# Kernel optimization log

Hardware: AMD Instinct MI355X
Metric: run time of the kernel (lower is better)

## Reference

```python
import jax, jax.numpy as jnp
import numpy as np

N_QUBITS = 8
N_LAYERS = 2
CDT = jnp.complex64


def _apply_1q(state, U, w):
    # state: [B] + [2]*n complex; U: [B,2,2] complex; acts on wire w (axis w+1)
    s = jnp.moveaxis(state, w + 1, -1)
    s = jnp.einsum('b...i,bji->b...j', s, U)
    return jnp.moveaxis(s, -1, w + 1)


def _rx(theta):
    t = theta * 0.5
    c, s = jnp.cos(t).astype(CDT), jnp.sin(t).astype(CDT)
    return jnp.stack([jnp.stack([c, -1j * s], -1), jnp.stack([-1j * s, c], -1)], -2)


def _ry(theta):
    t = theta * 0.5
    c, s = jnp.cos(t).astype(CDT), jnp.sin(t).astype(CDT)
    return jnp.stack([jnp.stack([c, -s], -1), jnp.stack([s, c], -1)], -2)


def _rz(theta):
    e = jnp.exp(-0.5j * theta.astype(CDT))
    z = jnp.zeros_like(e)
    return jnp.stack([jnp.stack([e, z], -1), jnp.stack([z, jnp.conj(e)], -1)], -2)


def _cnot(state, c, t):
    # control wire c, target wire t (c < t in this circuit) -> axes c+1, t+1
    s0 = jnp.take(state, jnp.array([0]), axis=c + 1)
    s1 = jnp.take(state, jnp.array([1]), axis=c + 1)
    s1 = jnp.flip(s1, axis=t + 1)
    return jnp.concatenate([s0, s1], axis=c + 1)


def _circuit(x, params):
    n, L = N_QUBITS, N_LAYERS
    B = x.shape[0]
    state = jnp.zeros((B,) + (2,) * n, CDT).at[(slice(None),) + (0,) * n].set(1.0)
    # data encoding: RY(x_i * pi), per-sample angles
    for i in range(n):
        state = _apply_1q(state, _ry(x[:, i] * jnp.pi), i)
    n_rot, n_ent = 3 * n, n * (n - 1) // 2
    for l in range(L):
        base = l * (n_rot + n_ent)
        rot = params[base:base + n_rot]
        ent = params[base + n_rot:base + n_rot + n_ent]
        for i in range(n):
            state = _apply_1q(state, _rx(jnp.broadcast_to(rot[3 * i], (B,))), i)
            state = _apply_1q(state, _ry(jnp.broadcast_to(rot[3 * i + 1], (B,))), i)
            state = _apply_1q(state, _rz(jnp.broadcast_to(rot[3 * i + 2], (B,))), i)
        k = 0
        for i in range(n):
            for j in range(i + 1, n):
                state = _cnot(state, i, j)
                state = _apply_1q(state, _rz(jnp.broadcast_to(ent[k], (B,))), j)
                k += 1
    probs = state.real ** 2 + state.imag ** 2  # [B] + [2]*n
    ev = []
    for w in range(n):
        p = jnp.moveaxis(probs, w + 1, 1).reshape(B, 2, -1).sum(-1)
        ev.append(p[:, 0] - p[:, 1])  # <Z_w>
    return jnp.stack(ev, -1)  # [B, n_qubits]


def setup_inputs() -> dict:
    key = jax.random.key(0)
    k1, k2, k3, k4 = jax.random.split(key, 4)
    B, n, C = 4096, N_QUBITS, 10
    x = jax.random.uniform(k1, (B, n), dtype=jnp.float32)
    params = jax.random.normal(k2, (104,), dtype=jnp.float32) * 0.1
    W = jax.random.normal(k3, (C, n), dtype=jnp.float32) * (1.0 / np.sqrt(n))
    b = jax.random.normal(k4, (C,), dtype=jnp.float32) * 0.01
    return {"x": x, "params": params, "W": W, "b": b}


def reference(x, params, W, b):
    quantum_out = _circuit(x, params)          # [B, n_qubits]
    return quantum_out @ W.T + b               # Linear post-process, [B, n_classes]
```

## Files before the change

kernel.cpp:

```cpp
#include <hip/hip_runtime.h>


#define PI_HALF 1.57079632679489662f

__device__ __forceinline__ float shfx(float v, int m)      { return __shfl_xor(v, m, 64); }
__device__ __forceinline__ float shfl_from(float v, int l) { return __shfl(v, l, 64); }
__device__ __forceinline__ float rdlane(float v, int l) {
    return __int_as_float(__builtin_amdgcn_readlane(__float_as_int(v), l));
}
__device__ __forceinline__ float sgnterm(float th, int pword) {
    return __int_as_float(__float_as_int(-th) ^ (int)((unsigned)pword << 31));
}

__global__ __launch_bounds__(256) void vqc_fused(
    const float* __restrict__ x,
    const float* __restrict__ prm,
    const float* __restrict__ W,
    const float* __restrict__ bvec,
    float* __restrict__ out)
{
    const int lane = threadIdx.x & 63;
    const int bi = __builtin_amdgcn_readfirstlane((blockIdx.x << 2) + (threadIdx.x >> 6));

    float mar, mai, mbr, mbi;
    {
        const int t = lane & 15;
        const int l = t >> 3, q = t & 7;
        const float* p3 = prm + l * 52 + 3 * q;
        float cx, sx, cy, sy, cz, sz;
        __sincosf(p3[0] * 0.5f, &sx, &cx);
        __sincosf(p3[1] * 0.5f, &sy, &cy);
        __sincosf(p3[2] * 0.5f, &sz, &cz);
        float n00r =  cy * cx, n00i =  sy * sx;
        float n01r = -sy * cx, n01i = -cy * sx;
        mar = cz * n00r + sz * n00i;
        mai = cz * n00i - sz * n00r;
        mbr = cz * n01r + sz * n01i;
        mbi = cz * n01i - sz * n01r;
    }

    float cw[8], swv[8];
    {
        const float4 x0 = ((const float4*)(x + bi * 8))[0];
        const float4 x1 = ((const float4*)(x + bi * 8))[1];
        float xv[8] = {x0.x, x0.y, x0.z, x0.w, x1.x, x1.y, x1.z, x1.w};
        #pragma unroll
        for (int w = 0; w < 8; ++w)
            __sincosf(xv[w] * PI_HALF, &swv[w], &cw[w]);
    }
    float base = 1.f;
    #pragma unroll
    for (int w = 0; w < 6; ++w)
        base *= ((lane >> (5 - w)) & 1) ? swv[w] : cw[w];
    float re[4], im[4];
    re[0] = base * cw[6]  * cw[7];  re[1] = base * cw[6]  * swv[7];
    re[2] = base * swv[6] * cw[7];  re[3] = base * swv[6] * swv[7];
    im[0] = im[1] = im[2] = im[3] = 0.f;

    int lb[6];
    #pragma unroll
    for (int b = 0; b < 6; ++b) lb[b] = lane >> b;

    const int pr = __popc(lane) & 1;
    int g = lane; g ^= g >> 1; g ^= g >> 2; g ^= g >> 4;
    const int src_lane = g;

    #pragma unroll
    for (int l = 0; l < 2; ++l) {
        #pragma unroll
        for (int i = 0; i < 8; ++i) {
            const int srcl = l * 8 + i;
            const float ar  = rdlane(mar, srcl);
            const float ai  = rdlane(mai, srcl);
            const float br  = rdlane(mbr, srcl);
            const float bi_ = rdlane(mbi, srcl);
            const int p = 7 - i;
            if (p >= 2) {
                const int mk = 1 << (p - 2);
                const int h  = (lane >> (p - 2)) & 1;
                const float Ai = h ? -ai : ai;
                const float Br = h ? -br : br;
                #pragma unroll
                for (int r = 0; r < 4; ++r) {
                    float pre = shfx(re[r], mk), pim = shfx(im[r], mk);
                    float cr = re[r], ci = im[r];
                    re[r] = ar * cr - Ai * ci + Br * pre - bi_ * pim;
                    im[r] = ar * ci + Ai * cr + Br * pim + bi_ * pre;
                }
            } else if (p == 1) {
                #pragma unroll
                for (int r0i = 0; r0i < 2; ++r0i) {
                    const int i0 = r0i, i1 = r0i + 2;
                    float r0 = re[i0], i0v = im[i0], r1 = re[i1], i1v = im[i1];
                    re[i0] =  ar * r0 - ai * i0v + br * r1 - bi_ * i1v;
                    im[i0] =  ar * i0v + ai * r0 + br * i1v + bi_ * r1;
                    re[i1] = -br * r0 - bi_ * i0v + ar * r1 + ai * i1v;
                    im[i1] = -br * i0v + bi_ * r0 + ar * i1v - ai * r1;
                }
            } else {
                #pragma unroll
                for (int r0i = 0; r0i < 2; ++r0i) {
                    const int i0 = 2 * r0i, i1 = 2 * r0i + 1;
                    float r0 = re[i0], i0v = im[i0], r1 = re[i1], i1v = im[i1];
                    re[i0] =  ar * r0 - ai * i0v + br * r1 - bi_ * i1v;
                    im[i0] =  ar * i0v + ai * r0 + br * i1v + bi_ * r1;
                    re[i1] = -br * r0 - bi_ * i0v + ar * r1 + ai * i1v;
                    im[i1] = -br * i0v + bi_ * r0 + ar * i1v - ai * r1;
                }
            }
        }

        {
            const float* pb = prm + l * 52 + 24;
            float A = 0.f, B6 = 0.f, B7 = 0.f, T = 0.f;
            int k = 0;
            #pragma unroll
            for (int i = 0; i < 8; ++i) {
                #pragma unroll
                for (int j = i + 1; j < 8; ++j, ++k) {
                    const float th = pb[k];
                    if (j <= 5)      A  += sgnterm(th, lb[5 - i] ^ lb[5 - j]);
                    else if (i == 6) T   = th;
                    else if (j == 6) B6 += sgnterm(th, lb[5 - i]);
                    else             B7 += sgnterm(th, lb[5 - i]);
                }
            }
            const float AB  = A + B6, AmB = A - B6;
            const float BmT = B7 - T, BpT = B7 + T;
            float ph[4] = { 0.5f * (AB  + BmT), 0.5f * (AB  - BmT),
                            0.5f * (AmB + BpT), 0.5f * (AmB - BpT) };
            #pragma unroll
            for (int r = 0; r < 4; ++r) {
                float c, s;
                __sincosf(ph[r], &s, &c);
                float nr = c * re[r] - s * im[r];
                float ni = c * im[r] + s * re[r];
                re[r] = nr; im[r] = ni;
            }
        }

        if (l == 0) {
            float Bre[4], Bim[4];
            #pragma unroll
            for (int m = 0; m < 4; ++m) {
                Bre[m] = shfl_from(re[m], src_lane);
                Bim[m] = shfl_from(im[m], src_lane);
            }
            re[0] = pr ? Bre[3] : Bre[0];  im[0] = pr ? Bim[3] : Bim[0];
            re[1] = pr ? Bre[2] : Bre[1];  im[1] = pr ? Bim[2] : Bim[1];
            re[2] = pr ? Bre[0] : Bre[3];  im[2] = pr ? Bim[0] : Bim[3];
            re[3] = pr ? Bre[1] : Bre[2];  im[3] = pr ? Bim[1] : Bim[2];
        }
    }

    float p0 = re[0]*re[0] + im[0]*im[0];
    float p1 = re[1]*re[1] + im[1]*im[1];
    float p2 = re[2]*re[2] + im[2]*im[2];
    float p3 = re[3]*re[3] + im[3]*im[3];
    float psum = p0 + p1 + p2 + p3;

    float v = psum;
    #pragma unroll
    for (int m = 1; m < 64; m <<= 1) {
        float pp = shfx(v, m);
        v = (lane & m) ? (pp - v) : (v + pp);
    }
    float t6 = p0 + p1 - p2 - p3;  t6 = (lane & 1) ? -t6 : t6;
    float t7 = p0 - p1 - p2 + p3;
    #pragma unroll
    for (int m = 1; m < 64; m <<= 1) { t6 += shfx(t6, m); t7 += shfx(t7, m); }

    const float e0 = shfl_from(v, 32);
    const float e1 = shfl_from(v, 48);
    const float e2 = shfl_from(v, 24);
    const float e3 = shfl_from(v, 12);
    const float e4 = shfl_from(v, 6);
    const float e5 = shfl_from(v, 3);

    if (lane < 10) {
        const float* Wr = W + lane * 8;
        float acc = bvec[lane];
        acc += e0 * Wr[0] + e1 * Wr[1] + e2 * Wr[2] + e3 * Wr[3];
        acc += e4 * Wr[4] + e5 * Wr[5] + t6 * Wr[6] + t7 * Wr[7];
        out[bi * 10 + lane] = acc;
    }
}

extern "C" void kernel_launch(void* const* d_in, const int* in_sizes, int n_in,
                              void* d_out, int out_size, void* d_ws, size_t ws_size,
                              hipStream_t stream) {
    const float* x    = (const float*)d_in[0];
    const float* prm  = (const float*)d_in[1];
    const float* W    = (const float*)d_in[2];
    const float* bvec = (const float*)d_in[3];
    float* out = (float*)d_out;

    const int B = in_sizes[0] / 8;
    vqc_fused<<<B / 4, 256, 0, stream>>>(x, prm, W, bvec, out);
}
```

Measured before the change: 14.19 us.

## Process two samples per wavefront using packed FP32 complex arithmetic

Each wavefront now simulates two batch samples instead of one, so the grid is halved. Complex amplitudes are held as float2 pairs and the gate updates use v_pk_mul_f32/v_pk_fma_f32 inline asm with op_sel swizzles, doing real and imaginary parts in one instruction. Gate-matrix readlanes, parameter sin/cos and the entangling-phase setup are amortized over two samples. In exchange each thread uses more registers, and fewer blocks means less parallelism across the GPU.

```diff
diff --git a/kernel.cpp b/kernel.cpp
--- a/kernel.cpp
+++ b/kernel.cpp
@@ -1,15 +1,38 @@
 #include <hip/hip_runtime.h>
 
+
+typedef float v2f __attribute__((ext_vector_type(2)));
 
 #define PI_HALF 1.57079632679489662f
 
 __device__ __forceinline__ float shfx(float v, int m)      { return __shfl_xor(v, m, 64); }
 __device__ __forceinline__ float shfl_from(float v, int l) { return __shfl(v, l, 64); }
+__device__ __forceinline__ v2f shfx2(v2f z, int m) {
+    v2f r; r.x = shfx(z.x, m); r.y = shfx(z.y, m); return r;
+}
+__device__ __forceinline__ v2f shfl_from2(v2f z, int l) {
+    v2f r; r.x = shfl_from(z.x, l); r.y = shfl_from(z.y, l); return r;
+}
 __device__ __forceinline__ float rdlane(float v, int l) {
     return __int_as_float(__builtin_amdgcn_readlane(__float_as_int(v), l));
 }
 __device__ __forceinline__ float sgnterm(float th, int pword) {
     return __int_as_float(__float_as_int(-th) ^ (int)((unsigned)pword << 31));
+}
+
+__device__ __forceinline__ v2f pk_mul(v2f a, v2f b) {
+    v2f d; asm("v_pk_mul_f32 %0, %1, %2" : "=v"(d) : "v"(a), "v"(b)); return d;
+}
+__device__ __forceinline__ v2f pk_fma(v2f a, v2f b, v2f c) {
+    v2f d; asm("v_pk_fma_f32 %0, %1, %2, %3" : "=v"(d) : "v"(a), "v"(b), "v"(c)); return d;
+}
+__device__ __forceinline__ v2f pk_fma_sw1(v2f a, v2f b, v2f c) {
+    v2f d; asm("v_pk_fma_f32 %0, %1, %2, %3 op_sel:[0,1,0] op_sel_hi:[1,0,1]"
+               : "=v"(d) : "v"(a), "v"(b), "v"(c)); return d;
+}
+__device__ __forceinline__ v2f pk_fma_sw01(v2f a, v2f b, v2f c) {
+    v2f d; asm("v_pk_fma_f32 %0, %1, %2, %3 op_sel:[1,1,0] op_sel_hi:[0,0,1]"
+               : "=v"(d) : "v"(a), "v"(b), "v"(c)); return d;
 }
 
 __global__ __launch_bounds__(256) void vqc_fused(
@@ -20,7 +43,9 @@
     float* __restrict__ out)
 {
     const int lane = threadIdx.x & 63;
-    const int bi = __builtin_amdgcn_readfirstlane((blockIdx.x << 2) + (threadIdx.x >> 6));
+    const int wid  = __builtin_amdgcn_readfirstlane((int)(threadIdx.x >> 6));
+    const int bi0  = (blockIdx.x << 3) + (wid << 1);
+    const int bi1  = bi0 + 1;
 
     float mar, mai, mbr, mbi;
     {
@@ -39,23 +64,28 @@
         mbi = cz * n01i - sz * n01r;
     }
 
-    float cw[8], swv[8];
-    {
-        const float4 x0 = ((const float4*)(x + bi * 8))[0];
-        const float4 x1 = ((const float4*)(x + bi * 8))[1];
-        float xv[8] = {x0.x, x0.y, x0.z, x0.w, x1.x, x1.y, x1.z, x1.w};
+    const float4 xa0 = ((const float4*)(x + bi0 * 8))[0];
+    const float4 xa1 = ((const float4*)(x + bi0 * 8))[1];
+    const float4 xb0 = ((const float4*)(x + bi1 * 8))[0];
+    const float4 xb1 = ((const float4*)(x + bi1 * 8))[1];
+    const float xs[2][8] = {{xa0.x, xa0.y, xa0.z, xa0.w, xa1.x, xa1.y, xa1.z, xa1.w},
+                            {xb0.x, xb0.y, xb0.z, xb0.w, xb1.x, xb1.y, xb1.z, xb1.w}};
+    v2f z[2][4];
+    #pragma unroll
+    for (int e = 0; e < 2; ++e) {
+        float cwv[8], swv[8];
         #pragma unroll
         for (int w = 0; w < 8; ++w)
-            __sincosf(xv[w] * PI_HALF, &swv[w], &cw[w]);
-    }
-    float base = 1.f;
-    #pragma unroll
-    for (int w = 0; w < 6; ++w)
-        base *= ((lane >> (5 - w)) & 1) ? swv[w] : cw[w];
-    float re[4], im[4];
-    re[0] = base * cw[6]  * cw[7];  re[1] = base * cw[6]  * swv[7];
-    re[2] = base * swv[6] * cw[7];  re[3] = base * swv[6] * swv[7];
-    im[0] = im[1] = im[2] = im[3] = 0.f;
+            __sincosf(xs[e][w] * PI_HALF, &swv[w], &cwv[w]);
+        float base = 1.f;
+        #pragma unroll
+        for (int w = 0; w < 6; ++w)
+            base *= ((lane >> (5 - w)) & 1) ? swv[w] : cwv[w];
+        z[e][0] = v2f{base * cwv[6] * cwv[7], 0.f};
+        z[e][1] = v2f{base * cwv[6] * swv[7], 0.f};
+        z[e][2] = v2f{base * swv[6] * cwv[7], 0.f};
+        z[e][3] = v2f{base * swv[6] * swv[7], 0.f};
+    }
 
     int lb[6];
     #pragma unroll
@@ -80,32 +110,49 @@
                 const int h  = (lane >> (p - 2)) & 1;
                 const float Ai = h ? -ai : ai;
                 const float Br = h ? -br : br;
-                #pragma unroll
-                for (int r = 0; r < 4; ++r) {
-                    float pre = shfx(re[r], mk), pim = shfx(im[r], mk);
-                    float cr = re[r], ci = im[r];
-                    re[r] = ar * cr - Ai * ci + Br * pre - bi_ * pim;
-                    im[r] = ar * ci + Ai * cr + Br * pim + bi_ * pre;
-                }
-            } else if (p == 1) {
-                #pragma unroll
-                for (int r0i = 0; r0i < 2; ++r0i) {
-                    const int i0 = r0i, i1 = r0i + 2;
-                    float r0 = re[i0], i0v = im[i0], r1 = re[i1], i1v = im[i1];
-                    re[i0] =  ar * r0 - ai * i0v + br * r1 - bi_ * i1v;
-                    im[i0] =  ar * i0v + ai * r0 + br * i1v + bi_ * r1;
-                    re[i1] = -br * r0 - bi_ * i0v + ar * r1 + ai * i1v;
-                    im[i1] = -br * i0v + bi_ * r0 + ar * i1v - ai * r1;
+                const v2f P1 = {ar, ar};
+                const v2f P2 = {-Ai, Ai};
+                const v2f P3 = {Br, Br};
+                const v2f P4 = {-bi_, bi_};
+                #pragma unroll
+                for (int e = 0; e < 2; ++e) {
+                    #pragma unroll
+                    for (int r = 0; r < 4; ++r) {
+                        v2f zz = z[e][r];
+                        v2f pz = shfx2(zz, mk);
+                        v2f t = pk_mul(P1, zz);
+                        t = pk_fma_sw1(P2, zz, t);
+                        t = pk_fma(P3, pz, t);
+                        t = pk_fma_sw1(P4, pz, t);
+                        z[e][r] = t;
+                    }
                 }
             } else {
-                #pragma unroll
-                for (int r0i = 0; r0i < 2; ++r0i) {
-                    const int i0 = 2 * r0i, i1 = 2 * r0i + 1;
-                    float r0 = re[i0], i0v = im[i0], r1 = re[i1], i1v = im[i1];
-                    re[i0] =  ar * r0 - ai * i0v + br * r1 - bi_ * i1v;
-                    im[i0] =  ar * i0v + ai * r0 + br * i1v + bi_ * r1;
-                    re[i1] = -br * r0 - bi_ * i0v + ar * r1 + ai * i1v;
-                    im[i1] = -br * i0v + bi_ * r0 + ar * i1v - ai * r1;
+                const v2f P1 = {ar, ar};
+                const v2f P2 = {-ai, ai};
+                const v2f P3 = {br, br};
+                const v2f P4 = {-bi_, bi_};
+                const v2f Q1 = {-br, -br};
+                const int i0a = (p == 1) ? 0 : 0, i1a = (p == 1) ? 2 : 1;
+                const int i0b = (p == 1) ? 1 : 2, i1b = (p == 1) ? 3 : 3;
+                #pragma unroll
+                for (int e = 0; e < 2; ++e) {
+                    {
+                        v2f z0 = z[e][i0a], z1 = z[e][i1a];
+                        v2f t0 = pk_mul(P1, z0); t0 = pk_fma_sw1(P2, z0, t0);
+                        t0 = pk_fma(P3, z1, t0); t0 = pk_fma_sw1(P4, z1, t0);
+                        v2f t1 = pk_mul(Q1, z0); t1 = pk_fma_sw1(P4, z0, t1);
+                        t1 = pk_fma(P1, z1, t1); t1 = pk_fma_sw01(P2, z1, t1);
+                        z[e][i0a] = t0; z[e][i1a] = t1;
+                    }
+                    {
+                        v2f z0 = z[e][i0b], z1 = z[e][i1b];
+                        v2f t0 = pk_mul(P1, z0); t0 = pk_fma_sw1(P2, z0, t0);
+                        t0 = pk_fma(P3, z1, t0); t0 = pk_fma_sw1(P4, z1, t0);
+                        v2f t1 = pk_mul(Q1, z0); t1 = pk_fma_sw1(P4, z0, t1);
+                        t1 = pk_fma(P1, z1, t1); t1 = pk_fma_sw01(P2, z1, t1);
+                        z[e][i0b] = t0; z[e][i1b] = t1;
+                    }
                 }
             }
         }
@@ -127,62 +174,80 @@
             }
             const float AB  = A + B6, AmB = A - B6;
             const float BmT = B7 - T, BpT = B7 + T;
-            float ph[4] = { 0.5f * (AB  + BmT), 0.5f * (AB  - BmT),
-                            0.5f * (AmB + BpT), 0.5f * (AmB - BpT) };
+            const float ph[4] = { 0.5f * (AB  + BmT), 0.5f * (AB  - BmT),
+                                  0.5f * (AmB + BpT), 0.5f * (AmB - BpT) };
             #pragma unroll
             for (int r = 0; r < 4; ++r) {
                 float c, s;
                 __sincosf(ph[r], &s, &c);
-                float nr = c * re[r] - s * im[r];
-                float ni = c * im[r] + s * re[r];
-                re[r] = nr; im[r] = ni;
+                const v2f Cc = {c, c};
+                const v2f Cs = {-s, s};
+                #pragma unroll
+                for (int e = 0; e < 2; ++e) {
+                    v2f t = pk_mul(Cc, z[e][r]);
+                    z[e][r] = pk_fma_sw1(Cs, z[e][r], t);
+                }
             }
         }
 
         if (l == 0) {
-            float Bre[4], Bim[4];
             #pragma unroll
-            for (int m = 0; m < 4; ++m) {
-                Bre[m] = shfl_from(re[m], src_lane);
-                Bim[m] = shfl_from(im[m], src_lane);
-            }
-            re[0] = pr ? Bre[3] : Bre[0];  im[0] = pr ? Bim[3] : Bim[0];
-            re[1] = pr ? Bre[2] : Bre[1];  im[1] = pr ? Bim[2] : Bim[1];
-            re[2] = pr ? Bre[0] : Bre[3];  im[2] = pr ? Bim[0] : Bim[3];
-            re[3] = pr ? Bre[1] : Bre[2];  im[3] = pr ? Bim[1] : Bim[2];
+            for (int e = 0; e < 2; ++e) {
+                v2f B0 = shfl_from2(z[e][0], src_lane);
+                v2f B1 = shfl_from2(z[e][1], src_lane);
+                v2f B2 = shfl_from2(z[e][2], src_lane);
+                v2f B3 = shfl_from2(z[e][3], src_lane);
+                z[e][0] = v2f{pr ? B3.x : B0.x, pr ? B3.y : B0.y};
+                z[e][1] = v2f{pr ? B2.x : B1.x, pr ? B2.y : B1.y};
+                z[e][2] = v2f{pr ? B0.x : B3.x, pr ? B0.y : B3.y};
+                z[e][3] = v2f{pr ? B1.x : B2.x, pr ? B1.y : B2.y};
+            }
         }
     }
 
-    float p0 = re[0]*re[0] + im[0]*im[0];
-    float p1 = re[1]*re[1] + im[1]*im[1];
-    float p2 = re[2]*re[2] + im[2]*im[2];
-    float p3 = re[3]*re[3] + im[3]*im[3];
-    float psum = p0 + p1 + p2 + p3;
-
-    float v = psum;
+    float vA, vB, t6A, t6B, t7A, t7B;
+    #pragma unroll
+    for (int e = 0; e < 2; ++e) {
+        float p0 = z[e][0].x*z[e][0].x + z[e][0].y*z[e][0].y;
+        float p1 = z[e][1].x*z[e][1].x + z[e][1].y*z[e][1].y;
+        float p2 = z[e][2].x*z[e][2].x + z[e][2].y*z[e][2].y;
+        float p3 = z[e][3].x*z[e][3].x + z[e][3].y*z[e][3].y;
+        float ps = p0 + p1 + p2 + p3;
+        float t6 = p0 + p1 - p2 - p3;  t6 = (lane & 1) ? -t6 : t6;
+        float t7 = p0 - p1 - p2 + p3;
+        if (e == 0) { vA = ps; t6A = t6; t7A = t7; }
+        else        { vB = ps; t6B = t6; t7B = t7; }
+    }
+    v2f vv  = {vA, vB};
+    v2f t6v = {t6A, t6B};
+    v2f t7v = {t7A, t7B};
     #pragma unroll
     for (int m = 1; m < 64; m <<= 1) {
-        float pp = shfx(v, m);
-        v = (lane & m) ? (pp - v) : (v + pp);
-    }
-    float t6 = p0 + p1 - p2 - p3;  t6 = (lane & 1) ? -t6 : t6;
-    float t7 = p0 - p1 - p2 + p3;
-    #pragma unroll
-    for (int m = 1; m < 64; m <<= 1) { t6 += shfx(t6, m); t7 += shfx(t7, m); }
-
-    const float e0 = shfl_from(v, 32);
-    const float e1 = shfl_from(v, 48);
-    const float e2 = shfl_from(v, 24);
-    const float e3 = shfl_from(v, 12);
-    const float e4 = shfl_from(v, 6);
-    const float e5 = shfl_from(v, 3);
+        v2f pp = shfx2(vv, m);
+        const bool neg = lane & m;
+        vv.x = neg ? (pp.x - vv.x) : (vv.x + pp.x);
+        vv.y = neg ? (pp.y - vv.y) : (vv.y + pp.y);
+        t6v += shfx2(t6v, m);
+        t7v += shfx2(t7v, m);
+    }
+    const float e0A = shfl_from(vv.x, 32), e0B = shfl_from(vv.y, 32);
+    const float e1A = shfl_from(vv.x, 48), e1B = shfl_from(vv.y, 48);
+    const float e2A = shfl_from(vv.x, 24), e2B = shfl_from(vv.y, 24);
+    const float e3A = shfl_from(vv.x, 12), e3B = shfl_from(vv.y, 12);
+    const float e4A = shfl_from(vv.x,  6), e4B = shfl_from(vv.y,  6);
+    const float e5A = shfl_from(vv.x,  3), e5B = shfl_from(vv.y,  3);
 
     if (lane < 10) {
         const float* Wr = W + lane * 8;
-        float acc = bvec[lane];
-        acc += e0 * Wr[0] + e1 * Wr[1] + e2 * Wr[2] + e3 * Wr[3];
-        acc += e4 * Wr[4] + e5 * Wr[5] + t6 * Wr[6] + t7 * Wr[7];
-        out[bi * 10 + lane] = acc;
+        const float w0 = Wr[0], w1 = Wr[1], w2 = Wr[2], w3 = Wr[3];
+        const float w4 = Wr[4], w5 = Wr[5], w6 = Wr[6], w7 = Wr[7];
+        const float bv = bvec[lane];
+        float accA = bv + e0A*w0 + e1A*w1 + e2A*w2 + e3A*w3
+                        + e4A*w4 + e5A*w5 + t6v.x*w6 + t7v.x*w7;
+        float accB = bv + e0B*w0 + e1B*w1 + e2B*w2 + e3B*w3
+                        + e4B*w4 + e5B*w5 + t6v.y*w6 + t7v.y*w7;
+        out[bi0 * 10 + lane] = accA;
+        out[bi1 * 10 + lane] = accB;
     }
 }
 
@@ -196,5 +261,5 @@
     float* out = (float*)d_out;
 
     const int B = in_sizes[0] / 8;
-    vqc_fused<<<B / 4, 256, 0, stream>>>(x, prm, W, bvec, out);
-}
+    vqc_fused<<<B / 8, 256, 0, stream>>>(x, prm, W, bvec, out);
+}
```

After: 14.16 us. About the same (-0.2%).
